# Optimization experiments

Measured on AMD Instinct MI355X. Metric: run time of the kernel, lower is better.

The kernel has to match this reference:

```python
import jax, jax.numpy as jnp
import numpy as np

B, S, H = 16, 4096, 768
N_SENT = 32
HH = H // 2  # per-direction LSTM hidden
NUM_LAYERS = 2


def attn_pool(x, mask, Wp, bp, v):
    # x: [N, L, H]; torch Linear is x @ W.T + b
    scores = jnp.einsum('nlh,h->nl', jnp.tanh(jnp.einsum('nlh,gh->nlg', x, Wp) + bp), v)
    if mask is not None:
        scores = jnp.where(mask, scores, -jnp.inf)
    w = jax.nn.softmax(scores, axis=1)  # [N, L]
    pooled = jnp.einsum('nlh,nl->nh', x, w)
    return pooled, w


def lstm_dir(x, Wih, Whh, bih, bhh, reverse):
    # x: [B, T, In]; PyTorch gate order i, f, g, o
    xg = jnp.einsum('bti,gi->btg', x, Wih) + bih  # [B, T, 4*HH]
    Bn = x.shape[0]
    init = (jnp.zeros((Bn, HH), x.dtype), jnp.zeros((Bn, HH), x.dtype))

    def step(carry, xt):
        h, c = carry
        g = xt + jnp.einsum('bh,gh->bg', h, Whh) + bhh
        i, f, gg, o = jnp.split(g, 4, axis=-1)
        c = jax.nn.sigmoid(f) * c + jax.nn.sigmoid(i) * jnp.tanh(gg)
        h = jax.nn.sigmoid(o) * jnp.tanh(c)
        return (h, c), h

    _, hs = jax.lax.scan(step, init, jnp.swapaxes(xg, 0, 1), reverse=reverse)
    return jnp.swapaxes(hs, 0, 1)  # [B, T, HH], time-aligned


def bilstm(x, Wih, Whh, bih, bhh):
    h = x
    for l in range(NUM_LAYERS):
        f = lstm_dir(h, Wih[l, 0], Whh[l, 0], bih[l, 0], bhh[l, 0], False)
        b = lstm_dir(h, Wih[l, 1], Whh[l, 1], bih[l, 1], bhh[l, 1], True)
        h = jnp.concatenate([f, b], axis=-1)  # [B, T, H]
    return h


def setup_inputs() -> dict:
    key = jax.random.key(0)
    ks = jax.random.split(key, 12)
    std = 0.02
    return {
        'hidden_states': jax.random.normal(ks[0], (B, S, H), jnp.float32),
        'attention_mask': jnp.ones((B, S), jnp.bool_),
        'w_proj_w': jax.random.normal(ks[1], (H, H), jnp.float32) * std,
        'w_proj_b': jnp.zeros((H,), jnp.float32),
        'w_vec': jax.random.normal(ks[2], (H,), jnp.float32) * std,
        'lstm_Wih': jax.random.normal(ks[3], (NUM_LAYERS, 2, 4 * HH, H), jnp.float32) * std,
        'lstm_Whh': jax.random.normal(ks[4], (NUM_LAYERS, 2, 4 * HH, HH), jnp.float32) * std,
        'lstm_bih': jnp.zeros((NUM_LAYERS, 2, 4 * HH), jnp.float32),
        'lstm_bhh': jnp.zeros((NUM_LAYERS, 2, 4 * HH), jnp.float32),
        's_proj_w': jax.random.normal(ks[5], (H, H), jnp.float32) * std,
        's_proj_b': jnp.zeros((H,), jnp.float32),
        's_vec': jax.random.normal(ks[6], (H,), jnp.float32) * std,
        'n_sent': N_SENT,
    }


def reference(hidden_states, attention_mask, w_proj_w, w_proj_b, w_vec,
              lstm_Wih, lstm_Whh, lstm_bih, lstm_bhh,
              s_proj_w, s_proj_b, s_vec, n_sent):
    b, s, h = hidden_states.shape
    L = s // n_sent
    # uniform sentence segmentation (boundaries at k*L-1): vectorized word attention
    x = hidden_states.reshape(b * n_sent, L, h)
    m = attention_mask.reshape(b * n_sent, L)
    pooled, w_attn = attn_pool(x, m, w_proj_w, w_proj_b, w_vec)  # [b*n_sent, h]
    sent = pooled.reshape(b, n_sent, h)
    enc = bilstm(sent, lstm_Wih, lstm_Whh, lstm_bih, lstm_bhh)  # [b, n_sent, h]
    doc, s_attn = attn_pool(enc, None, s_proj_w, s_proj_b, s_vec)  # [b, h]
    return doc, w_attn.reshape(b, n_sent, L), s_attn
```

## Files before the change

### kernel.cpp

```cpp
#include <hip/hip_runtime.h>
#include <math.h>

#define NB     16
#define NSENT  32
#define LW     128
#define HD     768
#define HH     384
#define NG     1536
#define NROWS  (NB*NSENT)
#define MW     (NROWS*LW)

typedef unsigned short ushort_t;
typedef unsigned long long u64;
typedef __attribute__((ext_vector_type(8))) short bf16x8;
typedef __attribute__((ext_vector_type(4))) float f32x4;
typedef __attribute__((ext_vector_type(4))) unsigned short u16x4;
typedef __attribute__((ext_vector_type(4))) unsigned int u32x4;

#define MFMA_BF16(a, b, c) __builtin_amdgcn_mfma_f32_16x16x32_bf16((a), (b), (c), 0, 0, 0)

__device__ __forceinline__ ushort_t f2bf(float x) {
  union { float f; unsigned u; } v; v.f = x;
  unsigned r = v.u + 0x7FFFu + ((v.u >> 16) & 1u);
  return (ushort_t)(r >> 16);
}
__device__ __forceinline__ float bf2f(ushort_t b) {
  union { unsigned u; float f; } v; v.u = ((unsigned)b) << 16; return v.f;
}
__device__ __forceinline__ float tanh_fast(float x) {
  float e = __builtin_amdgcn_exp2f(x * 2.88539008177793f);
  return 1.0f - 2.0f * __builtin_amdgcn_rcpf(e + 1.0f);
}
__device__ __forceinline__ float sigm(float x) {
  float e = __builtin_amdgcn_exp2f(-x * 1.44269504088896f);
  return __builtin_amdgcn_rcpf(1.0f + e);
}
__device__ __forceinline__ bf16x8 cvt8(float4 x, float4 y) {
  union { unsigned u[4]; bf16x8 v; } o;
  asm("v_cvt_pk_bf16_f32 %0, %1, %2" : "=v"(o.u[0]) : "v"(x.x), "v"(x.y));
  asm("v_cvt_pk_bf16_f32 %0, %1, %2" : "=v"(o.u[1]) : "v"(x.z), "v"(x.w));
  asm("v_cvt_pk_bf16_f32 %0, %1, %2" : "=v"(o.u[2]) : "v"(y.x), "v"(y.y));
  asm("v_cvt_pk_bf16_f32 %0, %1, %2" : "=v"(o.u[3]) : "v"(y.z), "v"(y.w));
  return o.v;
}
__device__ __forceinline__ void gload16(const void* g, void* l) {
  __builtin_amdgcn_global_load_lds(
      (const __attribute__((address_space(1))) unsigned int*)g,
      (__attribute__((address_space(3))) unsigned int*)l, 16, 0, 0);
}
__device__ __forceinline__ u64 ld64_ic(const u64* p) {
  return __hip_atomic_load(p, __ATOMIC_RELAXED, __HIP_MEMORY_SCOPE_AGENT);
}
__device__ __forceinline__ void st32_ic(unsigned* p, unsigned v) {
  __hip_atomic_store(p, v, __ATOMIC_RELAXED, __HIP_MEMORY_SCOPE_AGENT);
}
__device__ __forceinline__ bool bad64(u64 v) {
  return ((unsigned)v == 0xFFFFFFFFu) | ((unsigned)(v >> 32) == 0xFFFFFFFFu);
}

__global__ __launch_bounds__(256) void prologue_kernel(
    const float* __restrict__ wpw, const float* __restrict__ spw,
    const float* __restrict__ Wih, const float* __restrict__ Whh,
    const float* __restrict__ bih, const float* __restrict__ bhh,
    const float* __restrict__ hs,
    ushort_t* __restrict__ wp_bf, ushort_t* __restrict__ sp_bf,
    ushort_t* __restrict__ wih_bf, ushort_t* __restrict__ whh_bf,
    float* __restrict__ biasc, unsigned* __restrict__ hslots,
    ushort_t* __restrict__ hs_bf)
{
  const int gsz = gridDim.x * blockDim.x;
  const int gid = blockIdx.x * blockDim.x + threadIdx.x;
  auto cvt_seg = [&](const float* in, ushort_t* out, int n8) {
    for (int i = gid; i < n8; i += gsz) {
      const float4* p = (const float4*)(in + (size_t)i * 8);
      float4 a = p[0], b = p[1];
      *(bf16x8*)(out + (size_t)i * 8) = cvt8(a, b);
    }
  };
  cvt_seg(wpw, wp_bf, HD * HD / 8);
  cvt_seg(spw, sp_bf, HD * HD / 8);
  cvt_seg(Wih, wih_bf, 4 * NG * HD / 8);
  cvt_seg(Whh, whh_bf, 4 * NG * HH / 8);
  for (int i = gid; i < 4 * NG; i += gsz) biasc[i] = bih[i] + bhh[i];
  for (int i = gid; i < 2 * 2 * NSENT * 3072 / 4; i += gsz)
    *(u32x4*)(hslots + (size_t)i * 4) =
        (u32x4){0xFFFFFFFFu, 0xFFFFFFFFu, 0xFFFFFFFFu, 0xFFFFFFFFu};
  cvt_seg(hs, hs_bf, (int)((size_t)MW * HD / 8));
}

__global__ __launch_bounds__(512, 2) void score_big_kernel(
    const ushort_t* __restrict__ Ab, const ushort_t* __restrict__ W,
    const float* __restrict__ bias, const float* __restrict__ vvec,
    float* __restrict__ outp, int Mtotal)
{
  __shared__ __align__(16) char smem[122880];
  short* Albuf = (short*)smem;
  short* Blbuf = (short*)(smem + 49152);
  float* pbuf  = (float*)smem;

  const int tid = threadIdx.x;
  const int g = blockIdx.x;
  const int x = g & 7, s0 = g >> 3;
  const int nc = s0 & 3;
  const int m0 = (x + 8 * (s0 >> 2)) * 128;
  const int n0 = nc * 192;

  const unsigned wbase = (unsigned)(tid & ~63) * 16;

  const int w = tid >> 6, wr = w >> 2, wc = w & 3;
  const int l = tid & 63, lm = l & 15, lg = l >> 4;
  int arow[4], ar7[4];
  #pragma unroll
  for (int mt = 0; mt < 4; ++mt) { arow[mt] = wr * 64 + mt * 16 + lm; ar7[mt] = arow[mt] & 7; }
  int brow[3], br7[3];
  #pragma unroll
  for (int nt = 0; nt < 3; ++nt) { brow[nt] = wc * 48 + nt * 16 + lm; br7[nt] = brow[nt] & 7; }

  f32x4 acc[4][3];
  #pragma unroll
  for (int mt = 0; mt < 4; ++mt)
    #pragma unroll
    for (int nt = 0; nt < 3; ++nt) acc[mt][nt] = (f32x4){0.f, 0.f, 0.f, 0.f};

  const int a0r = tid >> 3,          a0u = (tid & 7) ^ (a0r & 7);
  const int a1r = (tid + 512) >> 3,  a1u = (tid & 7) ^ (a1r & 7);
  const int b2r = (tid + 1024) >> 3, b2u = (tid & 7) ^ (b2r & 7);

  auto stage = [&](int buf, int s) {
    const int kc = s * 64;
    char* Ad = (char*)Albuf + buf * 16384;
    char* Bd = (char*)Blbuf + buf * 24576;
    gload16(Ab + (size_t)(m0 + a0r) * HD + kc + a0u * 8, Ad + wbase);
    gload16(Ab + (size_t)(m0 + a1r) * HD + kc + a1u * 8, Ad + 8192 + wbase);
    gload16(W + (size_t)(n0 + a0r) * HD + kc + a0u * 8, Bd + wbase);
    gload16(W + (size_t)(n0 + a1r) * HD + kc + a1u * 8, Bd + 8192 + wbase);
    gload16(W + (size_t)(n0 + b2r) * HD + kc + b2u * 8, Bd + 16384 + wbase);
  };
  auto compute = [&](int buf) {
    const short* Asrc = Albuf + buf * 8192;
    const short* Bsrc = Blbuf + buf * 12288;
    #pragma unroll
    for (int kk = 0; kk < 2; ++kk) {
      const int u = kk * 4 + lg;
      bf16x8 af[4], bfr[3];
      #pragma unroll
      for (int mt = 0; mt < 4; ++mt)
        af[mt] = *(const bf16x8*)((const char*)Asrc + (unsigned)((arow[mt] * 8 + (u ^ ar7[mt])) << 4));
      #pragma unroll
      for (int nt = 0; nt < 3; ++nt)
        bfr[nt] = *(const bf16x8*)((const char*)Bsrc + (unsigned)((brow[nt] * 8 + (u ^ br7[nt])) << 4));
      #pragma unroll
      for (int mt = 0; mt < 4; ++mt)
        #pragma unroll
        for (int nt = 0; nt < 3; ++nt)
          acc[mt][nt] = MFMA_BF16(af[mt], bfr[nt], acc[mt][nt]);
    }
  };

  stage(0, 0);
  stage(1, 1);
  #pragma unroll
  for (int s = 0; s < 12; ++s) {
    if (s + 2 < 12) stage((s + 2) % 3, s + 2);
    if (s <= 9)       asm volatile("s_waitcnt vmcnt(10)" ::: "memory");
    else if (s == 10) asm volatile("s_waitcnt vmcnt(5)" ::: "memory");
    else              asm volatile("s_waitcnt vmcnt(0)" ::: "memory");
    __builtin_amdgcn_sched_barrier(0);
    __builtin_amdgcn_s_barrier();
    __builtin_amdgcn_sched_barrier(0);
    compute(s % 3);
    __builtin_amdgcn_sched_barrier(0);
    __builtin_amdgcn_s_barrier();
  }

  float sp[16];
  #pragma unroll
  for (int e = 0; e < 16; ++e) sp[e] = 0.f;
  #pragma unroll
  for (int nt = 0; nt < 3; ++nt) {
    const int col = n0 + wc * 48 + nt * 16 + lm;
    const float bb = bias[col], vv = vvec[col];
    #pragma unroll
    for (int mt = 0; mt < 4; ++mt)
      #pragma unroll
      for (int r = 0; r < 4; ++r)
        sp[mt * 4 + r] += tanh_fast(acc[mt][nt][r] + bb) * vv;
  }
  #pragma unroll
  for (int msk = 1; msk < 16; msk <<= 1)
    #pragma unroll
    for (int e = 0; e < 16; ++e) sp[e] += __shfl_xor(sp[e], msk, 64);
  if (lm == 0) {
    #pragma unroll
    for (int mt = 0; mt < 4; ++mt)
      #pragma unroll
      for (int r = 0; r < 4; ++r)
        pbuf[(wr * 4 + wc) * 64 + mt * 16 + lg * 4 + r] = sp[mt * 4 + r];
  }
  __syncthreads();
  if (tid < 128) {
    const int wrr = tid >> 6, idx = tid & 63;
    float ssum = pbuf[(wrr * 4 + 0) * 64 + idx] + pbuf[(wrr * 4 + 1) * 64 + idx]
               + pbuf[(wrr * 4 + 2) * 64 + idx] + pbuf[(wrr * 4 + 3) * 64 + idx];
    outp[(size_t)nc * Mtotal + m0 + wrr * 64 + idx] = ssum;
  }
}

template<int EPI>
__global__ __launch_bounds__(512, 2) void gemm_small_kernel(
    const ushort_t* __restrict__ Ab, const ushort_t* __restrict__ W,
    const float* __restrict__ bias, const float* __restrict__ vvec,
    float* __restrict__ outp, int Mtotal, int Ntot)
{
  __shared__ __align__(16) char smem[81920];
  short* Albuf = (short*)smem;
  short* Blbuf = (short*)(smem + 32768);
  float* pbuf  = (float*)smem;

  const int tid = threadIdx.x;
  const int nc = blockIdx.x;
  const int m0 = blockIdx.y * 128;
  const int n0 = nc * 192;

  const int rowA = tid >> 3, uA = tid & 7;
  const unsigned ubase = (unsigned)(uA ^ (rowA & 7));
  const unsigned soff = (unsigned)((rowA * 8 + ubase) * 16);

  const int w = tid >> 6, wr = w >> 2, wc = w & 3;
  const int l = tid & 63, lm = l & 15, lg = l >> 4;
  int arow[4], ar7[4];
  #pragma unroll
  for (int mt = 0; mt < 4; ++mt) { arow[mt] = wr * 64 + mt * 16 + lm; ar7[mt] = arow[mt] & 7; }
  int brow[3], br7[3];
  #pragma unroll
  for (int nt = 0; nt < 3; ++nt) { brow[nt] = wc * 48 + nt * 16 + lm; br7[nt] = brow[nt] & 7; }

  f32x4 acc[4][3];
  #pragma unroll
  for (int mt = 0; mt < 4; ++mt)
    #pragma unroll
    for (int nt = 0; nt < 3; ++nt) acc[mt][nt] = (f32x4){0.f, 0.f, 0.f, 0.f};

  bf16x8 a8[2]; bf16x8 b8[3];

  auto issue = [&](int s) {
    const int kc = s * 64 + uA * 8;
    const ushort_t* ap = Ab + (size_t)(m0 + rowA) * HD + kc;
    a8[0] = *(const bf16x8*)(ap);
    a8[1] = *(const bf16x8*)(ap + (size_t)64 * HD);
    #pragma unroll
    for (int i = 0; i < 3; ++i)
      b8[i] = *(const bf16x8*)(W + (size_t)(n0 + rowA + 64 * i) * HD + kc);
  };
  auto commit = [&](int buf) {
    short* Ad = Albuf + buf * 8192;
    short* Bd = Blbuf + buf * 12288;
    *(bf16x8*)((char*)Ad + soff) = a8[0];
    *(bf16x8*)((char*)Ad + soff + 8192) = a8[1];
    #pragma unroll
    for (int i = 0; i < 3; ++i)
      *(bf16x8*)((char*)Bd + soff + (unsigned)i * 8192) = b8[i];
  };

  issue(0);
  commit(0);
  int cur = 0;
  for (int s = 0; s < 12; ++s) {
    __syncthreads();
    if (s < 11) issue(s + 1);
    const short* Asrc = Albuf + cur * 8192;
    const short* Bsrc = Blbuf + cur * 12288;
    #pragma unroll
    for (int kk = 0; kk < 2; ++kk) {
      const int u = kk * 4 + lg;
      bf16x8 af[4], bfr[3];
      #pragma unroll
      for (int mt = 0; mt < 4; ++mt)
        af[mt] = *(const bf16x8*)((const char*)Asrc + (unsigned)((arow[mt] * 8 + (u ^ ar7[mt])) << 4));
      #pragma unroll
      for (int nt = 0; nt < 3; ++nt)
        bfr[nt] = *(const bf16x8*)((const char*)Bsrc + (unsigned)((brow[nt] * 8 + (u ^ br7[nt])) << 4));
      #pragma unroll
      for (int mt = 0; mt < 4; ++mt)
        #pragma unroll
        for (int nt = 0; nt < 3; ++nt)
          acc[mt][nt] = MFMA_BF16(af[mt], bfr[nt], acc[mt][nt]);
    }
    if (s < 11) commit(cur ^ 1);
    cur ^= 1;
  }

  if constexpr (EPI == 0) {
    float sp[16];
    #pragma unroll
    for (int e = 0; e < 16; ++e) sp[e] = 0.f;
    #pragma unroll
    for (int nt = 0; nt < 3; ++nt) {
      const int col = n0 + wc * 48 + nt * 16 + lm;
      const float bb = bias[col], vv = vvec[col];
      #pragma unroll
      for (int mt = 0; mt < 4; ++mt)
        #pragma unroll
        for (int r = 0; r < 4; ++r)
          sp[mt * 4 + r] += tanh_fast(acc[mt][nt][r] + bb) * vv;
    }
    #pragma unroll
    for (int msk = 1; msk < 16; msk <<= 1)
      #pragma unroll
      for (int e = 0; e < 16; ++e) sp[e] += __shfl_xor(sp[e], msk, 64);
    __syncthreads();
    if (lm == 0) {
      #pragma unroll
      for (int mt = 0; mt < 4; ++mt)
        #pragma unroll
        for (int r = 0; r < 4; ++r)
          pbuf[(wr * 4 + wc) * 64 + mt * 16 + lg * 4 + r] = sp[mt * 4 + r];
    }
    __syncthreads();
    if (tid < 128) {
      const int wrr = tid >> 6, idx = tid & 63;
      float ssum = pbuf[(wrr * 4 + 0) * 64 + idx] + pbuf[(wrr * 4 + 1) * 64 + idx]
                 + pbuf[(wrr * 4 + 2) * 64 + idx] + pbuf[(wrr * 4 + 3) * 64 + idx];
      outp[(size_t)nc * Mtotal + m0 + wrr * 64 + idx] = ssum;
    }
  } else {
    #pragma unroll
    for (int nt = 0; nt < 3; ++nt) {
      const int col = n0 + wc * 48 + nt * 16 + lm;
      const float bb = bias[col];
      #pragma unroll
      for (int mt = 0; mt < 4; ++mt) {
        const int mrow = m0 + wr * 64 + mt * 16 + lg * 4;
        #pragma unroll
        for (int r = 0; r < 4; ++r)
          outp[(size_t)(mrow + r) * Ntot + col] = acc[mt][nt][r] + bb;
      }
    }
  }
}

__global__ __launch_bounds__(64) void softmax128_kernel(const float* __restrict__ sc,
                                                        float* __restrict__ wout) {
  const int row = blockIdx.x, lane = threadIdx.x;
  float a = sc[row * 128 + lane]          + sc[MW + row * 128 + lane]
          + sc[2 * MW + row * 128 + lane] + sc[3 * MW + row * 128 + lane];
  float b = sc[row * 128 + 64 + lane]          + sc[MW + row * 128 + 64 + lane]
          + sc[2 * MW + row * 128 + 64 + lane] + sc[3 * MW + row * 128 + 64 + lane];
  float mx = fmaxf(a, b);
  #pragma unroll
  for (int m = 1; m < 64; m <<= 1) mx = fmaxf(mx, __shfl_xor(mx, m, 64));
  float ea = __builtin_amdgcn_exp2f((a - mx) * 1.44269504088896f);
  float eb = __builtin_amdgcn_exp2f((b - mx) * 1.44269504088896f);
  float s = ea + eb;
  #pragma unroll
  for (int m = 1; m < 64; m <<= 1) s += __shfl_xor(s, m, 64);
  float inv = 1.0f / s;
  wout[row * 128 + lane] = ea * inv;
  wout[row * 128 + 64 + lane] = eb * inv;
}

__global__ __launch_bounds__(192) void pool_kernel(
    const ushort_t* __restrict__ xbf, const float* __restrict__ wattn,
    ushort_t* __restrict__ pooledbf)
{
  __shared__ float wl[128];
  const int n = blockIdx.x, tid = threadIdx.x;
  if (tid < 128) wl[tid] = wattn[n * 128 + tid];
  __syncthreads();
  const ushort_t* xb = xbf + (size_t)n * LW * HD + tid * 4;
  float a0 = 0, a1 = 0, a2 = 0, a3 = 0;
  float b0 = 0, b1 = 0, b2 = 0, b3 = 0;
  for (int lq = 0; lq < LW; lq += 2) {
    u16x4 v0 = *(const u16x4*)(xb + (size_t)lq * HD);
    u16x4 v1 = *(const u16x4*)(xb + (size_t)(lq + 1) * HD);
    float w0 = wl[lq], w1 = wl[lq + 1];
    a0 += w0 * bf2f(v0[0]); a1 += w0 * bf2f(v0[1]);
    a2 += w0 * bf2f(v0[2]); a3 += w0 * bf2f(v0[3]);
    b0 += w1 * bf2f(v1[0]); b1 += w1 * bf2f(v1[1]);
    b2 += w1 * bf2f(v1[2]); b3 += w1 * bf2f(v1[3]);
  }
  u16x4 o;
  o[0] = f2bf(a0 + b0); o[1] = f2bf(a1 + b1); o[2] = f2bf(a2 + b2); o[3] = f2bf(a3 + b3);
  *(u16x4*)(pooledbf + (size_t)n * HD + tid * 4) = o;
}

__global__ __launch_bounds__(384) void lstm_kernel(
    const ushort_t* __restrict__ whh_l,
    const float* __restrict__ xg,
    unsigned* __restrict__ hb32,
    ushort_t* __restrict__ encbf)
{
  __shared__ __align__(16) short h_lds[16 * HH];
  __shared__ float gatebuf[16][100];
  __shared__ float cst[16][24];
  const int tid = threadIdx.x;
  const int d = blockIdx.x >> 4, cid = blockIdx.x & 15;
  const int w = tid >> 6, l = tid & 63, lm = l & 15, lg = l >> 4;
  const int b = tid / 24, jj = tid % 24, gj = cid * 24 + jj;

  bf16x8 wf[12];
  {
    int r = w * 16 + lm;
    int qq = r / 24, jjr = r % 24;
    const ushort_t* src = whh_l + ((size_t)d * NG + qq * HH + cid * 24 + jjr) * HH + lg * 8;
    #pragma unroll
    for (int kk = 0; kk < 12; ++kk) wf[kk] = *(const bf16x8*)(src + kk * 32);
  }
  cst[b][jj] = 0.f;
  __syncthreads();

  const int hr = tid / 24, hc = tid % 24;
  const int hu = hc * 2, hx = hr & 7;

  for (int t = 0; t < NSENT; ++t) {
    const int trev = d ? (NSENT - 1 - t) : t;
    const float* xp = xg + (size_t)(b * NSENT + trev) * 3072 + d * NG + gj;
    float xi = xp[0], xf = xp[HH], xgg = xp[2 * HH], xo = xp[3 * HH];

    f32x4 acc = (f32x4){0.f, 0.f, 0.f, 0.f};
    if (t > 0) {
      const u64* src = (const u64*)hb32 + (size_t)(d * NSENT + (t - 1)) * 1536 + hr * 96 + hc * 4;
      u64 v0, v1, v2, v3;
      for (;;) {
        v0 = ld64_ic(src + 0); v1 = ld64_ic(src + 1);
        v2 = ld64_ic(src + 2); v3 = ld64_ic(src + 3);
        if (!(bad64(v0) | bad64(v1) | bad64(v2) | bad64(v3))) break;
        __builtin_amdgcn_s_sleep(1);
      }
      u32x4 lo = (u32x4){(unsigned)v0, (unsigned)(v0 >> 32), (unsigned)v1, (unsigned)(v1 >> 32)};
      u32x4 hi = (u32x4){(unsigned)v2, (unsigned)(v2 >> 32), (unsigned)v3, (unsigned)(v3 >> 32)};
      *(u32x4*)((char*)h_lds + (unsigned)((hr * 48 + ((hu    ) ^ hx)) * 16)) = lo;
      *(u32x4*)((char*)h_lds + (unsigned)((hr * 48 + ((hu + 1) ^ hx)) * 16)) = hi;
      __syncthreads();

      #pragma unroll
      for (int kk = 0; kk < 12; ++kk) {
        bf16x8 a = *(const bf16x8*)((char*)h_lds +
                      (unsigned)((lm * 48 + ((kk * 4 + lg) ^ (lm & 7))) * 16));
        acc = MFMA_BF16(a, wf[kk], acc);
      }
    }
    #pragma unroll
    for (int r = 0; r < 4; ++r)
      gatebuf[lg * 4 + r][w * 16 + lm] = acc[r];
    __syncthreads();

    {
      float gi = gatebuf[b][jj]      + xi;
      float gf = gatebuf[b][24 + jj] + xf;
      float gg = gatebuf[b][48 + jj] + xgg;
      float go = gatebuf[b][72 + jj] + xo;
      float c = sigm(gf) * cst[b][jj] + sigm(gi) * tanh_fast(gg);
      float h = sigm(go) * tanh_fast(c);
      cst[b][jj] = c;
      unsigned hv = (unsigned)f2bf(h);
      unsigned up = __shfl_down(hv, 1);
      if ((jj & 1) == 0 && t < NSENT - 1)
        st32_ic(hb32 + (size_t)(d * NSENT + t) * 3072 + b * 192 + gj / 2, hv | (up << 16));
      encbf[((size_t)b * NSENT + trev) * HD + d * HH + gj] = f2bf(h);
    }
    __syncthreads();
  }
}

__global__ __launch_bounds__(64) void softmax32_kernel(const float* __restrict__ sc,
                                                       float* __restrict__ sattn,
                                                       float* __restrict__ sw) {
  const int b = blockIdx.x, lane = threadIdx.x;
  if (lane >= 32) return;
  float v = sc[b * 32 + lane]              + sc[NROWS + b * 32 + lane]
          + sc[2 * NROWS + b * 32 + lane]  + sc[3 * NROWS + b * 32 + lane];
  float mx = v;
  #pragma unroll
  for (int m = 1; m < 32; m <<= 1) mx = fmaxf(mx, __shfl_xor(mx, m, 32));
  float e = __builtin_amdgcn_exp2f((v - mx) * 1.44269504088896f);
  float s = e;
  #pragma unroll
  for (int m = 1; m < 32; m <<= 1) s += __shfl_xor(s, m, 32);
  float wv = e / s;
  sattn[b * 32 + lane] = wv;
  sw[b * 32 + lane] = wv;
}

__global__ __launch_bounds__(256) void doc_kernel(const ushort_t* __restrict__ enc2bf,
                                                  const float* __restrict__ sw,
                                                  float* __restrict__ doc) {
  __shared__ float wl[32];
  const int b = blockIdx.x, tid = threadIdx.x;
  if (tid < 32) wl[tid] = sw[b * 32 + tid];
  __syncthreads();
  for (int h = tid; h < HD; h += 256) {
    float a = 0.f;
    #pragma unroll
    for (int t = 0; t < 32; ++t)
      a += wl[t] * bf2f(enc2bf[((size_t)b * 32 + t) * HD + h]);
    doc[(size_t)b * HD + h] = a;
  }
}

extern "C" void kernel_launch(void* const* d_in, const int* in_sizes, int n_in,
                              void* d_out, int out_size, void* d_ws, size_t ws_size,
                              hipStream_t stream) {
  const float* hs  = (const float*)d_in[0];
  const float* wpw = (const float*)d_in[2];
  const float* wpb = (const float*)d_in[3];
  const float* wv  = (const float*)d_in[4];
  const float* Wih = (const float*)d_in[5];
  const float* Whh = (const float*)d_in[6];
  const float* bih = (const float*)d_in[7];
  const float* bhh = (const float*)d_in[8];
  const float* spw = (const float*)d_in[9];
  const float* spb = (const float*)d_in[10];
  const float* sv  = (const float*)d_in[11];

  float* out   = (float*)d_out;
  float* doc   = out;
  float* wattn = out + NB * HD;
  float* sattn = out + NB * HD + NROWS * LW;

  char* p = (char*)d_ws;
  auto take = [&p](size_t bytes) { char* q = p; p += (bytes + 255) & ~(size_t)255; return q; };
  ushort_t* wp_bf   = (ushort_t*)take((size_t)HD * HD * 2);
  ushort_t* sp_bf   = (ushort_t*)take((size_t)HD * HD * 2);
  ushort_t* wih_bf  = (ushort_t*)take((size_t)4 * NG * HD * 2);
  ushort_t* whh_bf  = (ushort_t*)take((size_t)4 * NG * HH * 2);
  float*    biasc   = (float*)take((size_t)4 * NG * 4);
  float*    wscore4 = (float*)take((size_t)4 * MW * 4);
  ushort_t* pooledbf= (ushort_t*)take((size_t)NROWS * HD * 2);
  float*    xgbuf   = (float*)take((size_t)NROWS * 2 * NG * 4);
  unsigned* hslots  = (unsigned*)take((size_t)2 * 2 * NSENT * 3072 * 4);
  ushort_t* enc1_bf = (ushort_t*)take((size_t)NROWS * HD * 2);
  ushort_t* enc2_bf = (ushort_t*)take((size_t)NROWS * HD * 2);
  float*    sscore4 = (float*)take((size_t)4 * NROWS * 4);
  float*    sw      = (float*)take((size_t)NB * NSENT * 4);
  ushort_t* hs_bf   = (ushort_t*)take((size_t)MW * HD * 2);

  prologue_kernel<<<2048, 256, 0, stream>>>(
      wpw, spw, Wih, Whh, bih, bhh, hs,
      wp_bf, sp_bf, wih_bf, whh_bf, biasc, hslots, hs_bf);

  score_big_kernel<<<dim3(2048), 512, 0, stream>>>(
      hs_bf, wp_bf, wpb, wv, wscore4, MW);
  softmax128_kernel<<<NROWS, 64, 0, stream>>>(wscore4, wattn);
  pool_kernel<<<NROWS, 192, 0, stream>>>(hs_bf, wattn, pooledbf);

  gemm_small_kernel<1><<<dim3(16, NROWS / 128), 512, 0, stream>>>(
      pooledbf, wih_bf, biasc, nullptr, xgbuf, NROWS, 2 * NG);
  {
    const ushort_t* a0 = whh_bf; const float* a1 = xgbuf; unsigned* a2 = hslots;
    ushort_t* a3 = enc1_bf;
    void* args[] = { &a0, &a1, &a2, &a3 };
    hipLaunchCooperativeKernel((void*)lstm_kernel, dim3(32), dim3(384), args, 0, stream);
  }
  gemm_small_kernel<1><<<dim3(16, NROWS / 128), 512, 0, stream>>>(
      enc1_bf, wih_bf + (size_t)2 * NG * HD, biasc + 2 * NG, nullptr,
      xgbuf, NROWS, 2 * NG);
  {
    const ushort_t* a0 = whh_bf + (size_t)2 * NG * HH; const float* a1 = xgbuf;
    unsigned* a2 = hslots + (size_t)2 * NSENT * 3072;
    ushort_t* a3 = enc2_bf;
    void* args[] = { &a0, &a1, &a2, &a3 };
    hipLaunchCooperativeKernel((void*)lstm_kernel, dim3(32), dim3(384), args, 0, stream);
  }

  gemm_small_kernel<0><<<dim3(4, NROWS / 128), 512, 0, stream>>>(
      enc2_bf, sp_bf, spb, sv, sscore4, NROWS, HD);
  softmax32_kernel<<<NB, 64, 0, stream>>>(sscore4, sattn, sw);
  doc_kernel<<<NB, 256, 0, stream>>>(enc2_bf, sw, doc);
}
```

Measured before the change: 386.1 us.

## Fuse fp32-to-bf16 conversion of hidden states into score GEMM A-tile loads

```diff
diff --git a/kernel.cpp b/kernel.cpp
--- a/kernel.cpp
+++ b/kernel.cpp
@@ -62,11 +62,9 @@
     const float* __restrict__ wpw, const float* __restrict__ spw,
     const float* __restrict__ Wih, const float* __restrict__ Whh,
     const float* __restrict__ bih, const float* __restrict__ bhh,
-    const float* __restrict__ hs,
     ushort_t* __restrict__ wp_bf, ushort_t* __restrict__ sp_bf,
     ushort_t* __restrict__ wih_bf, ushort_t* __restrict__ whh_bf,
-    float* __restrict__ biasc, unsigned* __restrict__ hslots,
-    ushort_t* __restrict__ hs_bf)
+    float* __restrict__ biasc, unsigned* __restrict__ hslots)
 {
   const int gsz = gridDim.x * blockDim.x;
   const int gid = blockIdx.x * blockDim.x + threadIdx.x;
@@ -85,11 +83,10 @@
   for (int i = gid; i < 2 * 2 * NSENT * 3072 / 4; i += gsz)
     *(u32x4*)(hslots + (size_t)i * 4) =
         (u32x4){0xFFFFFFFFu, 0xFFFFFFFFu, 0xFFFFFFFFu, 0xFFFFFFFFu};
-  cvt_seg(hs, hs_bf, (int)((size_t)MW * HD / 8));
 }
 
 __global__ __launch_bounds__(512, 2) void score_big_kernel(
-    const ushort_t* __restrict__ Ab, const ushort_t* __restrict__ W,
+    const float* __restrict__ Af, const ushort_t* __restrict__ W,
     const float* __restrict__ bias, const float* __restrict__ vvec,
     float* __restrict__ outp, int Mtotal)
 {
@@ -126,15 +123,39 @@
   const int a1r = (tid + 512) >> 3,  a1u = (tid & 7) ^ (a1r & 7);
   const int b2r = (tid + 1024) >> 3, b2u = (tid & 7) ^ (b2r & 7);
 
-  auto stage = [&](int buf, int s) {
+  float4 eA0, eA1, eA2, eA3;
+  float4 oA0, oA1, oA2, oA3;
+
+  auto issueB = [&](int buf, int s) {
     const int kc = s * 64;
-    char* Ad = (char*)Albuf + buf * 16384;
     char* Bd = (char*)Blbuf + buf * 24576;
-    gload16(Ab + (size_t)(m0 + a0r) * HD + kc + a0u * 8, Ad + wbase);
-    gload16(Ab + (size_t)(m0 + a1r) * HD + kc + a1u * 8, Ad + 8192 + wbase);
     gload16(W + (size_t)(n0 + a0r) * HD + kc + a0u * 8, Bd + wbase);
     gload16(W + (size_t)(n0 + a1r) * HD + kc + a1u * 8, Bd + 8192 + wbase);
     gload16(W + (size_t)(n0 + b2r) * HD + kc + b2u * 8, Bd + 16384 + wbase);
+  };
+  auto issueAe = [&](int s) {
+    const int kc = s * 64;
+    const float* p0 = Af + (size_t)(m0 + a0r) * HD + kc + a0u * 8;
+    const float* p1 = Af + (size_t)(m0 + a1r) * HD + kc + a1u * 8;
+    eA0 = *(const float4*)(p0); eA1 = *(const float4*)(p0 + 4);
+    eA2 = *(const float4*)(p1); eA3 = *(const float4*)(p1 + 4);
+  };
+  auto issueAo = [&](int s) {
+    const int kc = s * 64;
+    const float* p0 = Af + (size_t)(m0 + a0r) * HD + kc + a0u * 8;
+    const float* p1 = Af + (size_t)(m0 + a1r) * HD + kc + a1u * 8;
+    oA0 = *(const float4*)(p0); oA1 = *(const float4*)(p0 + 4);
+    oA2 = *(const float4*)(p1); oA3 = *(const float4*)(p1 + 4);
+  };
+  auto commitAe = [&](int buf) {
+    char* Ad = (char*)Albuf + buf * 16384;
+    *(bf16x8*)(Ad + (unsigned)tid * 16) = cvt8(eA0, eA1);
+    *(bf16x8*)(Ad + 8192 + (unsigned)tid * 16) = cvt8(eA2, eA3);
+  };
+  auto commitAo = [&](int buf) {
+    char* Ad = (char*)Albuf + buf * 16384;
+    *(bf16x8*)(Ad + (unsigned)tid * 16) = cvt8(oA0, oA1);
+    *(bf16x8*)(Ad + 8192 + (unsigned)tid * 16) = cvt8(oA2, oA3);
   };
   auto compute = [&](int buf) {
     const short* Asrc = Albuf + buf * 8192;
@@ -157,20 +178,35 @@
     }
   };
 
-  stage(0, 0);
-  stage(1, 1);
-  #pragma unroll
-  for (int s = 0; s < 12; ++s) {
-    if (s + 2 < 12) stage((s + 2) % 3, s + 2);
-    if (s <= 9)       asm volatile("s_waitcnt vmcnt(10)" ::: "memory");
-    else if (s == 10) asm volatile("s_waitcnt vmcnt(5)" ::: "memory");
-    else              asm volatile("s_waitcnt vmcnt(0)" ::: "memory");
-    __builtin_amdgcn_sched_barrier(0);
-    __builtin_amdgcn_s_barrier();
-    __builtin_amdgcn_sched_barrier(0);
-    compute(s % 3);
-    __builtin_amdgcn_sched_barrier(0);
-    __builtin_amdgcn_s_barrier();
+  issueAe(0); issueB(0, 0); commitAe(0);
+  issueAo(1); issueB(1, 1);
+  for (int s2 = 0; s2 < 12; s2 += 2) {
+    {
+      const int s = s2;
+      if (s + 2 < 12) { issueAe(s + 2); issueB((s + 2) % 3, s + 2); }
+      if (s + 1 < 12) commitAo((s + 1) % 3);
+      asm volatile("s_waitcnt lgkmcnt(0)" ::: "memory");
+      if (s == 11) asm volatile("s_waitcnt vmcnt(0)" ::: "memory");
+      __builtin_amdgcn_sched_barrier(0);
+      __builtin_amdgcn_s_barrier();
+      __builtin_amdgcn_sched_barrier(0);
+      compute(s % 3);
+      __builtin_amdgcn_sched_barrier(0);
+      __builtin_amdgcn_s_barrier();
+    }
+    {
+      const int s = s2 + 1;
+      if (s + 2 < 12) { issueAo(s + 2); issueB((s + 2) % 3, s + 2); }
+      if (s + 1 < 12) commitAe((s + 1) % 3);
+      asm volatile("s_waitcnt lgkmcnt(0)" ::: "memory");
+      if (s == 11) asm volatile("s_waitcnt vmcnt(0)" ::: "memory");
+      __builtin_amdgcn_sched_barrier(0);
+      __builtin_amdgcn_s_barrier();
+      __builtin_amdgcn_sched_barrier(0);
+      compute(s % 3);
+      __builtin_amdgcn_sched_barrier(0);
+      __builtin_amdgcn_s_barrier();
+    }
   }
 
   float sp[16];
@@ -223,8 +259,7 @@
   const int n0 = nc * 192;
 
   const int rowA = tid >> 3, uA = tid & 7;
-  const unsigned ubase = (unsigned)(uA ^ (rowA & 7));
-  const unsigned soff = (unsigned)((rowA * 8 + ubase) * 16);
+  const unsigned soff = (unsigned)((rowA * 8 + (uA ^ (rowA & 7))) * 16);
 
   const int w = tid >> 6, wr = w >> 2, wc = w & 3;
   const int l = tid & 63, lm = l & 15, lg = l >> 4;
@@ -339,45 +374,42 @@
   }
 }
 
-__global__ __launch_bounds__(64) void softmax128_kernel(const float* __restrict__ sc,
-                                                        float* __restrict__ wout) {
-  const int row = blockIdx.x, lane = threadIdx.x;
-  float a = sc[row * 128 + lane]          + sc[MW + row * 128 + lane]
-          + sc[2 * MW + row * 128 + lane] + sc[3 * MW + row * 128 + lane];
-  float b = sc[row * 128 + 64 + lane]          + sc[MW + row * 128 + 64 + lane]
-          + sc[2 * MW + row * 128 + 64 + lane] + sc[3 * MW + row * 128 + 64 + lane];
-  float mx = fmaxf(a, b);
-  #pragma unroll
-  for (int m = 1; m < 64; m <<= 1) mx = fmaxf(mx, __shfl_xor(mx, m, 64));
-  float ea = __builtin_amdgcn_exp2f((a - mx) * 1.44269504088896f);
-  float eb = __builtin_amdgcn_exp2f((b - mx) * 1.44269504088896f);
-  float s = ea + eb;
-  #pragma unroll
-  for (int m = 1; m < 64; m <<= 1) s += __shfl_xor(s, m, 64);
-  float inv = 1.0f / s;
-  wout[row * 128 + lane] = ea * inv;
-  wout[row * 128 + 64 + lane] = eb * inv;
-}
-
-__global__ __launch_bounds__(192) void pool_kernel(
-    const ushort_t* __restrict__ xbf, const float* __restrict__ wattn,
-    ushort_t* __restrict__ pooledbf)
+__global__ __launch_bounds__(192) void softpool_kernel(
+    const float* __restrict__ sc, const float* __restrict__ x,
+    float* __restrict__ wout, ushort_t* __restrict__ pooledbf)
 {
   __shared__ float wl[128];
   const int n = blockIdx.x, tid = threadIdx.x;
-  if (tid < 128) wl[tid] = wattn[n * 128 + tid];
+  if (tid < 64) {
+    const int lane = tid;
+    float a = sc[n * 128 + lane]          + sc[MW + n * 128 + lane]
+            + sc[2 * MW + n * 128 + lane] + sc[3 * MW + n * 128 + lane];
+    float b = sc[n * 128 + 64 + lane]          + sc[MW + n * 128 + 64 + lane]
+            + sc[2 * MW + n * 128 + 64 + lane] + sc[3 * MW + n * 128 + 64 + lane];
+    float mx = fmaxf(a, b);
+    #pragma unroll
+    for (int m = 1; m < 64; m <<= 1) mx = fmaxf(mx, __shfl_xor(mx, m, 64));
+    float ea = __builtin_amdgcn_exp2f((a - mx) * 1.44269504088896f);
+    float eb = __builtin_amdgcn_exp2f((b - mx) * 1.44269504088896f);
+    float s = ea + eb;
+    #pragma unroll
+    for (int m = 1; m < 64; m <<= 1) s += __shfl_xor(s, m, 64);
+    float inv = 1.0f / s;
+    wout[n * 128 + lane] = ea * inv;
+    wout[n * 128 + 64 + lane] = eb * inv;
+    wl[lane] = ea * inv;
+    wl[64 + lane] = eb * inv;
+  }
   __syncthreads();
-  const ushort_t* xb = xbf + (size_t)n * LW * HD + tid * 4;
+  const float* xb = x + (size_t)n * LW * HD + tid * 4;
   float a0 = 0, a1 = 0, a2 = 0, a3 = 0;
   float b0 = 0, b1 = 0, b2 = 0, b3 = 0;
   for (int lq = 0; lq < LW; lq += 2) {
-    u16x4 v0 = *(const u16x4*)(xb + (size_t)lq * HD);
-    u16x4 v1 = *(const u16x4*)(xb + (size_t)(lq + 1) * HD);
+    float4 v0 = *(const float4*)(xb + (size_t)lq * HD);
+    float4 v1 = *(const float4*)(xb + (size_t)(lq + 1) * HD);
     float w0 = wl[lq], w1 = wl[lq + 1];
-    a0 += w0 * bf2f(v0[0]); a1 += w0 * bf2f(v0[1]);
-    a2 += w0 * bf2f(v0[2]); a3 += w0 * bf2f(v0[3]);
-    b0 += w1 * bf2f(v1[0]); b1 += w1 * bf2f(v1[1]);
-    b2 += w1 * bf2f(v1[2]); b3 += w1 * bf2f(v1[3]);
+    a0 += w0 * v0.x; a1 += w0 * v0.y; a2 += w0 * v0.z; a3 += w0 * v0.w;
+    b0 += w1 * v1.x; b1 += w1 * v1.y; b2 += w1 * v1.z; b3 += w1 * v1.w;
   }
   u16x4 o;
   o[0] = f2bf(a0 + b0); o[1] = f2bf(a1 + b1); o[2] = f2bf(a2 + b2); o[3] = f2bf(a3 + b3);
@@ -420,12 +452,12 @@
     f32x4 acc = (f32x4){0.f, 0.f, 0.f, 0.f};
     if (t > 0) {
       const u64* src = (const u64*)hb32 + (size_t)(d * NSENT + (t - 1)) * 1536 + hr * 96 + hc * 4;
-      u64 v0, v1, v2, v3;
-      for (;;) {
+      u64 v0 = ld64_ic(src + 0), v1 = ld64_ic(src + 1);
+      u64 v2 = ld64_ic(src + 2), v3 = ld64_ic(src + 3);
+      while (bad64(v0) | bad64(v1) | bad64(v2) | bad64(v3)) {
+        __builtin_amdgcn_s_sleep(1);
         v0 = ld64_ic(src + 0); v1 = ld64_ic(src + 1);
         v2 = ld64_ic(src + 2); v3 = ld64_ic(src + 3);
-        if (!(bad64(v0) | bad64(v1) | bad64(v2) | bad64(v3))) break;
-        __builtin_amdgcn_s_sleep(1);
       }
       u32x4 lo = (u32x4){(unsigned)v0, (unsigned)(v0 >> 32), (unsigned)v1, (unsigned)(v1 >> 32)};
       u32x4 hi = (u32x4){(unsigned)v2, (unsigned)(v2 >> 32), (unsigned)v3, (unsigned)(v3 >> 32)};
@@ -463,31 +495,26 @@
   }
 }
 
-__global__ __launch_bounds__(64) void softmax32_kernel(const float* __restrict__ sc,
-                                                       float* __restrict__ sattn,
-                                                       float* __restrict__ sw) {
-  const int b = blockIdx.x, lane = threadIdx.x;
-  if (lane >= 32) return;
-  float v = sc[b * 32 + lane]              + sc[NROWS + b * 32 + lane]
-          + sc[2 * NROWS + b * 32 + lane]  + sc[3 * NROWS + b * 32 + lane];
-  float mx = v;
-  #pragma unroll
-  for (int m = 1; m < 32; m <<= 1) mx = fmaxf(mx, __shfl_xor(mx, m, 32));
-  float e = __builtin_amdgcn_exp2f((v - mx) * 1.44269504088896f);
-  float s = e;
-  #pragma unroll
-  for (int m = 1; m < 32; m <<= 1) s += __shfl_xor(s, m, 32);
-  float wv = e / s;
-  sattn[b * 32 + lane] = wv;
-  sw[b * 32 + lane] = wv;
-}
-
-__global__ __launch_bounds__(256) void doc_kernel(const ushort_t* __restrict__ enc2bf,
-                                                  const float* __restrict__ sw,
-                                                  float* __restrict__ doc) {
+__global__ __launch_bounds__(256) void smdoc_kernel(
+    const float* __restrict__ sc, const ushort_t* __restrict__ enc2bf,
+    float* __restrict__ sattn, float* __restrict__ doc)
+{
   __shared__ float wl[32];
   const int b = blockIdx.x, tid = threadIdx.x;
-  if (tid < 32) wl[tid] = sw[b * 32 + tid];
+  if (tid < 32) {
+    float v = sc[b * 32 + tid]              + sc[NROWS + b * 32 + tid]
+            + sc[2 * NROWS + b * 32 + tid]  + sc[3 * NROWS + b * 32 + tid];
+    float mx = v;
+    #pragma unroll
+    for (int m = 1; m < 32; m <<= 1) mx = fmaxf(mx, __shfl_xor(mx, m, 32));
+    float e = __builtin_amdgcn_exp2f((v - mx) * 1.44269504088896f);
+    float s = e;
+    #pragma unroll
+    for (int m = 1; m < 32; m <<= 1) s += __shfl_xor(s, m, 32);
+    float wv = e / s;
+    sattn[b * 32 + tid] = wv;
+    wl[tid] = wv;
+  }
   __syncthreads();
   for (int h = tid; h < HD; h += 256) {
     float a = 0.f;
@@ -532,17 +559,14 @@
   ushort_t* enc1_bf = (ushort_t*)take((size_t)NROWS * HD * 2);
   ushort_t* enc2_bf = (ushort_t*)take((size_t)NROWS * HD * 2);
   float*    sscore4 = (float*)take((size_t)4 * NROWS * 4);
-  float*    sw      = (float*)take((size_t)NB * NSENT * 4);
-  ushort_t* hs_bf   = (ushort_t*)take((size_t)MW * HD * 2);
-
-  prologue_kernel<<<2048, 256, 0, stream>>>(
-      wpw, spw, Wih, Whh, bih, bhh, hs,
-      wp_bf, sp_bf, wih_bf, whh_bf, biasc, hslots, hs_bf);
+
+  prologue_kernel<<<512, 256, 0, stream>>>(
+      wpw, spw, Wih, Whh, bih, bhh,
+      wp_bf, sp_bf, wih_bf, whh_bf, biasc, hslots);
 
   score_big_kernel<<<dim3(2048), 512, 0, stream>>>(
-      hs_bf, wp_bf, wpb, wv, wscore4, MW);
-  softmax128_kernel<<<NROWS, 64, 0, stream>>>(wscore4, wattn);
-  pool_kernel<<<NROWS, 192, 0, stream>>>(hs_bf, wattn, pooledbf);
+      hs, wp_bf, wpb, wv, wscore4, MW);
+  softpool_kernel<<<NROWS, 192, 0, stream>>>(wscore4, hs, wattn, pooledbf);
 
   gemm_small_kernel<1><<<dim3(16, NROWS / 128), 512, 0, stream>>>(
       pooledbf, wih_bf, biasc, nullptr, xgbuf, NROWS, 2 * NG);
@@ -565,6 +589,5 @@
 
   gemm_small_kernel<0><<<dim3(4, NROWS / 128), 512, 0, stream>>>(
       enc2_bf, sp_bf, spb, sv, sscore4, NROWS, HD);
-  softmax32_kernel<<<NB, 64, 0, stream>>>(sscore4, sattn, sw);
-  doc_kernel<<<NB, 256, 0, stream>>>(enc2_bf, sw, doc);
-}
+  smdoc_kernel<<<NB, 256, 0, stream>>>(sscore4, enc2_bf, sattn, doc);
+}
```

After: 373.9 us. -3.2%, faster.
